# Optimization experiments

Hardware: AMD Instinct MI355X
Metric: run time of the kernel (lower is better)

The kernel has to match this reference:

```python
import jax, jax.numpy as jnp
import numpy as np

X_WEIGHT = 1.0
Y_WEIGHT = 1.0


def setup_inputs() -> dict:
    key = jax.random.key(0)
    k1, k2 = jax.random.split(key)
    B, C, H, W = 32, 8, 256, 256
    inp = jax.random.normal(k1, (B, C, H, W), dtype=jnp.float32)
    tgt = jax.random.uniform(k2, (B, C, H, W), dtype=jnp.float32)
    return {"input": inp, "target": tgt}


def reference(input, target):
    B, C, H, W = input.shape
    # coordinate maps: x[j] = (j+1 - W/2)/W, y[p] = (p+1 - H/2)/H  (tanh half-range)
    xs = (jnp.arange(W, dtype=jnp.float32) + 1.0 - W / 2.0) / W  # [W]
    ys = (jnp.arange(H, dtype=jnp.float32) + 1.0 - H / 2.0) / H  # [H]

    # DSNT: softmax over each flattened heatmap, then coordinate expectation
    p = jax.nn.softmax(input.reshape(B, C, H * W), axis=-1).reshape(B, C, H, W)
    pred_x = jnp.einsum('bchw,w->bc', p, xs)  # [B, C]
    pred_y = jnp.einsum('bchw,h->bc', p, ys)  # [B, C]

    # ground truth via argmax of target heatmap, converted to same coord range
    idx = jnp.argmax(target.reshape(B, C, H * W), axis=-1)  # [B, C] int
    true_x = ((idx % W).astype(jnp.float32) + 1.0 - W / 2.0) / W
    true_y = ((idx // W).astype(jnp.float32) + 1.0 - H / 2.0) / H

    # per-heatmap MSE over the 2-vector (x, y), each weighted
    dx = pred_x * X_WEIGHT - true_x * X_WEIGHT
    dy = pred_y * Y_WEIGHT - true_y * Y_WEIGHT
    mse = 0.5 * (dx * dx + dy * dy)  # [B, C]

    # original sums over all B*C heatmaps, then divides by B (i+1 == batch size)
    return jnp.sum(mse) / B
```

## Files before the change

### kernel.cpp

```cpp
#include <hip/hip_runtime.h>
#include <math.h>

#define HW 65536
#define NMAPS 256
#define THREADS 256
#define CHUNKS 8
#define F4_PER_CHUNK 2048
#define F4_PER_THREAD 8

#define SHIFT_M 8.0f

__global__ __launch_bounds__(THREADS, 8) void dsnt_pass1(const float* __restrict__ input,
                                                         const float* __restrict__ target,
                                                         float4* __restrict__ wsA,
                                                         float2* __restrict__ wsB) {
    const int b    = blockIdx.x;
    const int role = b & 1;
    const int id   = b >> 1;
    const int map  = id >> 3;
    const int chunk = id & 7;
    const int tid  = threadIdx.x;
    const int wave = tid >> 6, lane = tid & 63;

    const float LOG2E  = 1.4426950408889634f;
    const float INV256 = 1.0f / 256.0f;
    const float NSH    = -SHIFT_M * LOG2E;

    __shared__ float red0[4], red1[4], red2[4];
    __shared__ int   red3[4];

    if (role == 0) {
        const float4* p = (const float4*)(input + (size_t)map * HW) + chunk * F4_PER_CHUNK;
        float4 v[F4_PER_THREAD];
#pragma unroll
        for (int k = 0; k < F4_PER_THREAD; ++k) v[k] = p[tid + k * THREADS];

        float s0 = 0.f, s1 = 0.f;
        float sx0 = 0.f, sx1 = 0.f;
        float sy0 = 0.f, sy1 = 0.f;
#pragma unroll
        for (int k = 0; k < F4_PER_THREAD; ++k) {
            int Q  = chunk * F4_PER_CHUNK + tid + k * THREADS;
            int h  = Q >> 6;
            int w0 = (Q & 63) << 2;
            float cy  = (float)(h  - 127) * INV256;
            float cx0 = (float)(w0 - 127) * INV256;
            float4 vv = v[k];

            float e0 = __builtin_exp2f(fmaf(vv.x, LOG2E, NSH));
            float e1 = __builtin_exp2f(fmaf(vv.y, LOG2E, NSH));
            float e2 = __builtin_exp2f(fmaf(vv.z, LOG2E, NSH));
            float e3 = __builtin_exp2f(fmaf(vv.w, LOG2E, NSH));
            float esum  = (e0 + e1) + (e2 + e3);
            float exsum = fmaf(e0, cx0,
                          fmaf(e1, cx0 + INV256,
                          fmaf(e2, cx0 + 2.f * INV256,
                               e3 * (cx0 + 3.f * INV256))));
            if (k & 1) { s1 += esum; sx1 += exsum; sy1 = fmaf(esum, cy, sy1); }
            else       { s0 += esum; sx0 += exsum; sy0 = fmaf(esum, cy, sy0); }
        }
        float s = s0 + s1, sx = sx0 + sx1, sy = sy0 + sy1;

#pragma unroll
        for (int k = 1; k < 64; k <<= 1) {
            s  += __shfl_xor(s,  k, 64);
            sx += __shfl_xor(sx, k, 64);
            sy += __shfl_xor(sy, k, 64);
        }
        if (lane == 0) { red0[wave] = s; red1[wave] = sx; red2[wave] = sy; }
        __syncthreads();
        if (tid == 0) {
            s  = (red0[0] + red0[1]) + (red0[2] + red0[3]);
            sx = (red1[0] + red1[1]) + (red1[2] + red1[3]);
            sy = (red2[0] + red2[1]) + (red2[2] + red2[3]);
            wsA[id] = make_float4(s, sx, sy, 0.f);
        }
    } else {
        const float4* p = (const float4*)(target + (size_t)map * HW) + chunk * F4_PER_CHUNK;
        float4 t[F4_PER_THREAD];
#pragma unroll
        for (int k = 0; k < F4_PER_THREAD; ++k) t[k] = p[tid + k * THREADS];

        float tv = -INFINITY;
        int   ti = 0x7fffffff;
#pragma unroll
        for (int k = 0; k < F4_PER_THREAD; ++k) {
            int Q  = chunk * F4_PER_CHUNK + tid + k * THREADS;
            int j0 = Q << 2;
            float4 tt = t[k];
            if (tt.x > tv) { tv = tt.x; ti = j0;     }
            if (tt.y > tv) { tv = tt.y; ti = j0 + 1; }
            if (tt.z > tv) { tv = tt.z; ti = j0 + 2; }
            if (tt.w > tv) { tv = tt.w; ti = j0 + 3; }
        }
#pragma unroll
        for (int k = 1; k < 64; k <<= 1) {
            float otv = __shfl_xor(tv, k, 64);
            int   oti = __shfl_xor(ti, k, 64);
            bool take = (otv > tv) || (otv == tv && oti < ti);
            tv = take ? otv : tv;
            ti = take ? oti : ti;
        }
        if (lane == 0) { red0[wave] = tv; red3[wave] = ti; }
        __syncthreads();
        if (tid == 0) {
            tv = red0[0]; ti = red3[0];
            for (int i = 1; i < 4; ++i) {
                float otv = red0[i]; int oti = red3[i];
                if (otv > tv || (otv == tv && oti < ti)) { tv = otv; ti = oti; }
            }
            wsB[id] = make_float2(tv, __int_as_float(ti));
        }
    }
}

__global__ __launch_bounds__(NMAPS) void dsnt_pass2(const float4* __restrict__ wsA,
                                                    const float2* __restrict__ wsB,
                                                    float* __restrict__ out) {
    const int t = threadIdx.x;
    const float INV256 = 1.0f / 256.0f;

    float s = 0.f, sx = 0.f, sy = 0.f;
    float tv = -INFINITY;
    int   ti = 0x7fffffff;
#pragma unroll
    for (int c = 0; c < CHUNKS; ++c) {
        float4 a = wsA[t * CHUNKS + c];
        s += a.x; sx += a.y; sy += a.z;
        float2 bb = wsB[t * CHUNKS + c];
        int oti = __float_as_int(bb.y);
        if (bb.x > tv || (bb.x == tv && oti < ti)) { tv = bb.x; ti = oti; }
    }
    float px = sx / s, py = sy / s;
    float tx = (float)((ti & 255) - 127) * INV256;
    float ty = (float)((ti >> 8)  - 127) * INV256;
    float dx = px - tx, dy = py - ty;
    float loss = 0.5f * (dx * dx + dy * dy);

#pragma unroll
    for (int k = 32; k > 0; k >>= 1) loss += __shfl_down(loss, k, 64);
    __shared__ float partial[4];
    int wave = t >> 6, lane = t & 63;
    if (lane == 0) partial[wave] = loss;
    __syncthreads();
    if (t == 0) {
        float total = (partial[0] + partial[1]) + (partial[2] + partial[3]);
        out[0] = total * (1.0f / 32.0f);
    }
}

extern "C" void kernel_launch(void* const* d_in, const int* in_sizes, int n_in,
                              void* d_out, int out_size, void* d_ws, size_t ws_size,
                              hipStream_t stream) {
    const float* input  = (const float*)d_in[0];
    const float* target = (const float*)d_in[1];
    float4* wsA = (float4*)d_ws;
    float2* wsB = (float2*)((char*)d_ws + 2048 * sizeof(float4));
    float*  out = (float*)d_out;

    dsnt_pass1<<<2 * 2048, THREADS, 0, stream>>>(input, target, wsA, wsB);
    dsnt_pass2<<<1, NMAPS, 0, stream>>>(wsA, wsB, out);
}
```

Baseline: 143.6 us.

## Use fewer, larger blocks with register double-buffered loads across two rounds

Each block now covers half a heatmap (8192 float4) instead of an eighth, so the grid drops from 4096 to 1024 blocks. Inside a block the loads are issued in rounds of 16 float4 per thread, and the next round's load is started as soon as a register slot has been consumed. This is meant to keep more loads in flight per thread and to cut per-block launch and reduction overhead. In exchange, register pressure rises and occupancy falls (launch bounds go from 8 to 4), and only 1024 blocks remain to spread across the GPU.

```diff
diff --git a/kernel.cpp b/kernel.cpp
--- a/kernel.cpp
+++ b/kernel.cpp
@@ -2,23 +2,23 @@
 #include <math.h>
 
 #define HW 65536
+#define F4_PER_MAP 16384
 #define NMAPS 256
 #define THREADS 256
-#define CHUNKS 8
-#define F4_PER_CHUNK 2048
-#define F4_PER_THREAD 8
+#define CHUNKS 2
+#define F4_PER_BLOCK 8192
+#define DEPTH 16
+#define ROUNDS 2
 
 #define SHIFT_M 8.0f
 
-__global__ __launch_bounds__(THREADS, 8) void dsnt_pass1(const float* __restrict__ input,
+__global__ __launch_bounds__(THREADS, 4) void dsnt_pass1(const float* __restrict__ input,
                                                          const float* __restrict__ target,
                                                          float4* __restrict__ wsA,
                                                          float2* __restrict__ wsB) {
     const int b    = blockIdx.x;
     const int role = b & 1;
     const int id   = b >> 1;
-    const int map  = id >> 3;
-    const int chunk = id & 7;
     const int tid  = threadIdx.x;
     const int wave = tid >> 6, lane = tid & 63;
 
@@ -30,34 +30,41 @@
     __shared__ int   red3[4];
 
     if (role == 0) {
-        const float4* p = (const float4*)(input + (size_t)map * HW) + chunk * F4_PER_CHUNK;
-        float4 v[F4_PER_THREAD];
+        const float4* p = (const float4*)input + (size_t)id * F4_PER_BLOCK;
+
+        float4 buf[DEPTH];
 #pragma unroll
-        for (int k = 0; k < F4_PER_THREAD; ++k) v[k] = p[tid + k * THREADS];
+        for (int k = 0; k < DEPTH; ++k) buf[k] = p[tid + k * THREADS];
 
-        float s0 = 0.f, s1 = 0.f;
-        float sx0 = 0.f, sx1 = 0.f;
-        float sy0 = 0.f, sy1 = 0.f;
+        float s0 = 0.f, s1 = 0.f, sx0 = 0.f, sx1 = 0.f, sy0 = 0.f, sy1 = 0.f;
+
 #pragma unroll
-        for (int k = 0; k < F4_PER_THREAD; ++k) {
-            int Q  = chunk * F4_PER_CHUNK + tid + k * THREADS;
-            int h  = Q >> 6;
-            int w0 = (Q & 63) << 2;
-            float cy  = (float)(h  - 127) * INV256;
-            float cx0 = (float)(w0 - 127) * INV256;
-            float4 vv = v[k];
+        for (int j = 0; j < ROUNDS; ++j) {
+#pragma unroll
+            for (int k = 0; k < DEPTH; ++k) {
+                float4 vv = buf[k];
+                if (j + 1 < ROUNDS)
+                    buf[k] = p[tid + ((j + 1) * DEPTH + k) * THREADS];
 
-            float e0 = __builtin_exp2f(fmaf(vv.x, LOG2E, NSH));
-            float e1 = __builtin_exp2f(fmaf(vv.y, LOG2E, NSH));
-            float e2 = __builtin_exp2f(fmaf(vv.z, LOG2E, NSH));
-            float e3 = __builtin_exp2f(fmaf(vv.w, LOG2E, NSH));
-            float esum  = (e0 + e1) + (e2 + e3);
-            float exsum = fmaf(e0, cx0,
-                          fmaf(e1, cx0 + INV256,
-                          fmaf(e2, cx0 + 2.f * INV256,
-                               e3 * (cx0 + 3.f * INV256))));
-            if (k & 1) { s1 += esum; sx1 += exsum; sy1 = fmaf(esum, cy, sy1); }
-            else       { s0 += esum; sx0 += exsum; sy0 = fmaf(esum, cy, sy0); }
+                int Q  = id * F4_PER_BLOCK + (j * DEPTH + k) * THREADS + tid;
+                int lq = Q & (F4_PER_MAP - 1);
+                int h  = lq >> 6;
+                int w0 = (lq & 63) << 2;
+                float cy  = (float)(h  - 127) * INV256;
+                float cx0 = (float)(w0 - 127) * INV256;
+
+                float e0 = __builtin_exp2f(fmaf(vv.x, LOG2E, NSH));
+                float e1 = __builtin_exp2f(fmaf(vv.y, LOG2E, NSH));
+                float e2 = __builtin_exp2f(fmaf(vv.z, LOG2E, NSH));
+                float e3 = __builtin_exp2f(fmaf(vv.w, LOG2E, NSH));
+                float esum  = (e0 + e1) + (e2 + e3);
+                float exsum = fmaf(e0, cx0,
+                              fmaf(e1, cx0 + INV256,
+                              fmaf(e2, cx0 + 2.f * INV256,
+                                   e3 * (cx0 + 3.f * INV256))));
+                if (k & 1) { s1 += esum; sx1 += exsum; sy1 = fmaf(esum, cy, sy1); }
+                else       { s0 += esum; sx0 += exsum; sy0 = fmaf(esum, cy, sy0); }
+            }
         }
         float s = s0 + s1, sx = sx0 + sx1, sy = sy0 + sy1;
 
@@ -76,22 +83,31 @@
             wsA[id] = make_float4(s, sx, sy, 0.f);
         }
     } else {
-        const float4* p = (const float4*)(target + (size_t)map * HW) + chunk * F4_PER_CHUNK;
-        float4 t[F4_PER_THREAD];
+        const float4* p = (const float4*)target + (size_t)id * F4_PER_BLOCK;
+
+        float4 buf[DEPTH];
 #pragma unroll
-        for (int k = 0; k < F4_PER_THREAD; ++k) t[k] = p[tid + k * THREADS];
+        for (int k = 0; k < DEPTH; ++k) buf[k] = p[tid + k * THREADS];
 
         float tv = -INFINITY;
         int   ti = 0x7fffffff;
+
 #pragma unroll
-        for (int k = 0; k < F4_PER_THREAD; ++k) {
-            int Q  = chunk * F4_PER_CHUNK + tid + k * THREADS;
-            int j0 = Q << 2;
-            float4 tt = t[k];
-            if (tt.x > tv) { tv = tt.x; ti = j0;     }
-            if (tt.y > tv) { tv = tt.y; ti = j0 + 1; }
-            if (tt.z > tv) { tv = tt.z; ti = j0 + 2; }
-            if (tt.w > tv) { tv = tt.w; ti = j0 + 3; }
+        for (int j = 0; j < ROUNDS; ++j) {
+#pragma unroll
+            for (int k = 0; k < DEPTH; ++k) {
+                float4 tt = buf[k];
+                if (j + 1 < ROUNDS)
+                    buf[k] = p[tid + ((j + 1) * DEPTH + k) * THREADS];
+
+                int Q  = id * F4_PER_BLOCK + (j * DEPTH + k) * THREADS + tid;
+                int lq = Q & (F4_PER_MAP - 1);
+                int j0 = lq << 2;
+                if (tt.x > tv) { tv = tt.x; ti = j0;     }
+                if (tt.y > tv) { tv = tt.y; ti = j0 + 1; }
+                if (tt.z > tv) { tv = tt.z; ti = j0 + 2; }
+                if (tt.w > tv) { tv = tt.w; ti = j0 + 3; }
+            }
         }
 #pragma unroll
         for (int k = 1; k < 64; k <<= 1) {
@@ -155,9 +171,9 @@
     const float* input  = (const float*)d_in[0];
     const float* target = (const float*)d_in[1];
     float4* wsA = (float4*)d_ws;
-    float2* wsB = (float2*)((char*)d_ws + 2048 * sizeof(float4));
+    float2* wsB = (float2*)((char*)d_ws + 512 * sizeof(float4));
     float*  out = (float*)d_out;
 
-    dsnt_pass1<<<2 * 2048, THREADS, 0, stream>>>(input, target, wsA, wsB);
+    dsnt_pass1<<<2 * 512, THREADS, 0, stream>>>(input, target, wsA, wsB);
     dsnt_pass2<<<1, NMAPS, 0, stream>>>(wsA, wsB, out);
 }
```

Result: slower. 146.7 us (+2.2%).

## Fuse final reduction via last-block atomic ticket and enlarge per-block chunks

Applied to the files above, without the earlier changes.

Merges the second-pass kernel into the first using an atomic counter so the last finishing block computes the final loss, removing one kernel launch. Also halves the number of chunks per map (16 float4 per thread) and switches to nontemporal streaming loads issued inside the loop. A memset is added to reset the counter each call, which adds its own launch-like cost, and the larger per-block work lowers the block count and may reduce latency hiding.

```diff
diff --git a/kernel.cpp b/kernel.cpp
--- a/kernel.cpp
+++ b/kernel.cpp
@@ -2,23 +2,30 @@
 #include <math.h>
 
 #define HW 65536
+#define F4_PER_MAP 16384
 #define NMAPS 256
 #define THREADS 256
-#define CHUNKS 8
-#define F4_PER_CHUNK 2048
-#define F4_PER_THREAD 8
+#define CHUNKS 4
+#define F4_PER_CHUNK 4096
+#define F4_PER_THREAD 16
+#define NIDS 1024
+#define NBLOCKS 2048
 
 #define SHIFT_M 8.0f
 
-__global__ __launch_bounds__(THREADS, 8) void dsnt_pass1(const float* __restrict__ input,
-                                                         const float* __restrict__ target,
-                                                         float4* __restrict__ wsA,
-                                                         float2* __restrict__ wsB) {
+typedef __attribute__((ext_vector_type(4))) float fvec4;
+
+__global__ __launch_bounds__(THREADS) void dsnt_fused(const float* __restrict__ input,
+                                                      const float* __restrict__ target,
+                                                      float4* __restrict__ wsA,
+                                                      float2* __restrict__ wsB,
+                                                      unsigned int* __restrict__ counter,
+                                                      float* __restrict__ out) {
     const int b    = blockIdx.x;
     const int role = b & 1;
     const int id   = b >> 1;
-    const int map  = id >> 3;
-    const int chunk = id & 7;
+    const int map  = id >> 2;
+    const int chunk = id & 3;
     const int tid  = threadIdx.x;
     const int wave = tid >> 6, lane = tid & 63;
 
@@ -28,24 +35,21 @@
 
     __shared__ float red0[4], red1[4], red2[4];
     __shared__ int   red3[4];
+    __shared__ unsigned int sticket;
+
+    const fvec4* p = (const fvec4*)(role == 0 ? input : target)
+                   + (size_t)map * F4_PER_MAP + chunk * F4_PER_CHUNK;
 
     if (role == 0) {
-        const float4* p = (const float4*)(input + (size_t)map * HW) + chunk * F4_PER_CHUNK;
-        float4 v[F4_PER_THREAD];
-#pragma unroll
-        for (int k = 0; k < F4_PER_THREAD; ++k) v[k] = p[tid + k * THREADS];
-
-        float s0 = 0.f, s1 = 0.f;
-        float sx0 = 0.f, sx1 = 0.f;
-        float sy0 = 0.f, sy1 = 0.f;
+        float s0 = 0.f, s1 = 0.f, sx0 = 0.f, sx1 = 0.f, sy0 = 0.f, sy1 = 0.f;
 #pragma unroll
         for (int k = 0; k < F4_PER_THREAD; ++k) {
-            int Q  = chunk * F4_PER_CHUNK + tid + k * THREADS;
+            fvec4 vv = __builtin_nontemporal_load(p + k * THREADS + tid);
+            int Q  = chunk * F4_PER_CHUNK + k * THREADS + tid;
             int h  = Q >> 6;
             int w0 = (Q & 63) << 2;
             float cy  = (float)(h  - 127) * INV256;
             float cx0 = (float)(w0 - 127) * INV256;
-            float4 vv = v[k];
 
             float e0 = __builtin_exp2f(fmaf(vv.x, LOG2E, NSH));
             float e1 = __builtin_exp2f(fmaf(vv.y, LOG2E, NSH));
@@ -60,7 +64,6 @@
             else       { s0 += esum; sx0 += exsum; sy0 = fmaf(esum, cy, sy0); }
         }
         float s = s0 + s1, sx = sx0 + sx1, sy = sy0 + sy1;
-
 #pragma unroll
         for (int k = 1; k < 64; k <<= 1) {
             s  += __shfl_xor(s,  k, 64);
@@ -76,18 +79,13 @@
             wsA[id] = make_float4(s, sx, sy, 0.f);
         }
     } else {
-        const float4* p = (const float4*)(target + (size_t)map * HW) + chunk * F4_PER_CHUNK;
-        float4 t[F4_PER_THREAD];
-#pragma unroll
-        for (int k = 0; k < F4_PER_THREAD; ++k) t[k] = p[tid + k * THREADS];
-
         float tv = -INFINITY;
         int   ti = 0x7fffffff;
 #pragma unroll
         for (int k = 0; k < F4_PER_THREAD; ++k) {
-            int Q  = chunk * F4_PER_CHUNK + tid + k * THREADS;
+            fvec4 tt = __builtin_nontemporal_load(p + k * THREADS + tid);
+            int Q  = chunk * F4_PER_CHUNK + k * THREADS + tid;
             int j0 = Q << 2;
-            float4 tt = t[k];
             if (tt.x > tv) { tv = tt.x; ti = j0;     }
             if (tt.y > tv) { tv = tt.y; ti = j0 + 1; }
             if (tt.z > tv) { tv = tt.z; ti = j0 + 2; }
@@ -112,40 +110,40 @@
             wsB[id] = make_float2(tv, __int_as_float(ti));
         }
     }
-}
 
-__global__ __launch_bounds__(NMAPS) void dsnt_pass2(const float4* __restrict__ wsA,
-                                                    const float2* __restrict__ wsB,
-                                                    float* __restrict__ out) {
-    const int t = threadIdx.x;
-    const float INV256 = 1.0f / 256.0f;
-
-    float s = 0.f, sx = 0.f, sy = 0.f;
-    float tv = -INFINITY;
-    int   ti = 0x7fffffff;
+    if (tid == 0) {
+        __threadfence();
+        sticket = atomicAdd(counter, 1u);
+    }
+    __syncthreads();
+    if (sticket == NBLOCKS - 1) {
+        __threadfence();
+        const int t = tid;
+        float s = 0.f, sx = 0.f, sy = 0.f;
+        float tv = -INFINITY;
+        int   ti = 0x7fffffff;
 #pragma unroll
-    for (int c = 0; c < CHUNKS; ++c) {
-        float4 a = wsA[t * CHUNKS + c];
-        s += a.x; sx += a.y; sy += a.z;
-        float2 bb = wsB[t * CHUNKS + c];
-        int oti = __float_as_int(bb.y);
-        if (bb.x > tv || (bb.x == tv && oti < ti)) { tv = bb.x; ti = oti; }
-    }
-    float px = sx / s, py = sy / s;
-    float tx = (float)((ti & 255) - 127) * INV256;
-    float ty = (float)((ti >> 8)  - 127) * INV256;
-    float dx = px - tx, dy = py - ty;
-    float loss = 0.5f * (dx * dx + dy * dy);
-
+        for (int c = 0; c < CHUNKS; ++c) {
+            float4 a = wsA[t * CHUNKS + c];
+            s += a.x; sx += a.y; sy += a.z;
+            float2 bb = wsB[t * CHUNKS + c];
+            int oti = __float_as_int(bb.y);
+            if (bb.x > tv || (bb.x == tv && oti < ti)) { tv = bb.x; ti = oti; }
+        }
+        float px = sx / s, py = sy / s;
+        float tx = (float)((ti & 255) - 127) * INV256;
+        float ty = (float)((ti >> 8)  - 127) * INV256;
+        float dx = px - tx, dy = py - ty;
+        float loss = 0.5f * (dx * dx + dy * dy);
 #pragma unroll
-    for (int k = 32; k > 0; k >>= 1) loss += __shfl_down(loss, k, 64);
-    __shared__ float partial[4];
-    int wave = t >> 6, lane = t & 63;
-    if (lane == 0) partial[wave] = loss;
-    __syncthreads();
-    if (t == 0) {
-        float total = (partial[0] + partial[1]) + (partial[2] + partial[3]);
-        out[0] = total * (1.0f / 32.0f);
+        for (int k = 32; k > 0; k >>= 1) loss += __shfl_down(loss, k, 64);
+        __syncthreads();
+        if (lane == 0) red0[wave] = loss;
+        __syncthreads();
+        if (tid == 0) {
+            float total = (red0[0] + red0[1]) + (red0[2] + red0[3]);
+            out[0] = total * (1.0f / 32.0f);
+        }
     }
 }
 
@@ -155,9 +153,10 @@
     const float* input  = (const float*)d_in[0];
     const float* target = (const float*)d_in[1];
     float4* wsA = (float4*)d_ws;
-    float2* wsB = (float2*)((char*)d_ws + 2048 * sizeof(float4));
-    float*  out = (float*)d_out;
+    float2* wsB = (float2*)((char*)d_ws + NIDS * sizeof(float4));
+    unsigned int* counter = (unsigned int*)((char*)d_ws + NIDS * (sizeof(float4) + sizeof(float2)));
+    float* out = (float*)d_out;
 
-    dsnt_pass1<<<2 * 2048, THREADS, 0, stream>>>(input, target, wsA, wsB);
-    dsnt_pass2<<<1, NMAPS, 0, stream>>>(wsA, wsB, out);
+    hipMemsetAsync(counter, 0, sizeof(unsigned int), stream);
+    dsnt_fused<<<NBLOCKS, THREADS, 0, stream>>>(input, target, wsA, wsB, counter, out);
 }
```

New measurement: 233.6 us. +62.6%, slower.
